# Optimization experiments

Measured on AMD Instinct MI355X. Metric: run time of the kernel, lower is better.

Reference implementation:

```python
import jax, jax.numpy as jnp
import numpy as np
import math

K_HISTORY = 32  # sliding-window length over GRU hidden states


def rotate_half(x):
    half = x.shape[-1] // 2
    return jnp.concatenate([-x[..., half:], x[..., :half]], axis=-1)


def setup_inputs() -> dict:
    key = jax.random.key(0)
    ks = jax.random.split(key, 8)
    B, MB, IN = 8, 512, 1024          # batch, max_bin, input_size (gru_hidden_size)
    EMB, H, KVH, HD, BS = 1024, 16, 4, 64, 16  # embed_dim, heads, kv_heads, head_dim, bin_size
    h = jax.random.normal(ks[0], (B, MB, IN), jnp.float32)
    # RoPE tables: rotate-half layout, theta repeated over both halves
    pos = jnp.arange(MB, dtype=jnp.float32)
    inv_freq = 1.0 / (10000.0 ** (jnp.arange(0, HD, 2, dtype=jnp.float32) / HD))
    theta = pos[:, None] * inv_freq[None, :]            # (MB, HD/2)
    theta = jnp.concatenate([theta, theta], axis=-1)    # (MB, HD)
    freqs_cos = jnp.cos(theta)
    freqs_sin = jnp.sin(theta)
    s = 0.02
    Wq = jax.random.normal(ks[1], (EMB, H * HD), jnp.float32) * s
    Wk = jax.random.normal(ks[2], (IN, KVH * HD), jnp.float32) * s
    Wv = jax.random.normal(ks[3], (IN, KVH * HD), jnp.float32) * s
    Wo = jax.random.normal(ks[4], (H * HD, EMB), jnp.float32) * s
    output_queries = jax.random.normal(ks[5], (BS, EMB), jnp.float32)
    Wr = jax.random.normal(ks[6], (EMB, 2), jnp.float32) * s
    br = jnp.zeros((2,), jnp.float32)
    return {"h": h, "freqs_cos": freqs_cos, "freqs_sin": freqs_sin,
            "Wq": Wq, "Wk": Wk, "Wv": Wv, "Wo": Wo,
            "output_queries": output_queries, "Wr": Wr, "br": br}


def reference(h, freqs_cos, freqs_sin, Wq, Wk, Wv, Wo, output_queries, Wr, br):
    B, MB, IN = h.shape
    HD = freqs_cos.shape[1]
    H = Wq.shape[1] // HD
    KVH = Wk.shape[1] // HD
    n_rep = H // KVH
    BS = output_queries.shape[0]
    K = K_HISTORY

    # sliding windows over bins: window t covers h[t-K+1 : t+1] (zero left-pad)
    h_padded = jnp.concatenate([jnp.zeros((B, K - 1, IN), h.dtype), h], axis=1)
    idx = jnp.arange(MB)[:, None] + jnp.arange(K)[None, :]   # (MB, K)
    h_win = h_padded[:, idx, :]                              # (B, MB, K, IN)

    k = (h_win @ Wk).reshape(B, MB, K, KVH, HD)
    v = (h_win @ Wv).reshape(B, MB, K, KVH, HD)

    # queries: shared learned output queries, identical across batch & bins
    q = (output_queries @ Wq).reshape(BS, H, HD)             # (BS, H, HD)
    # RoPE on Q only (is_decoder=True) at within-bin offsets 0..BS-1
    offs = jnp.arange(BS)
    cos = freqs_cos[offs][:, None, :]                        # (BS, 1, HD)
    sin = freqs_sin[offs][:, None, :]
    q = q * cos + rotate_half(q) * sin                       # (BS, H, HD)

    # GQA: repeat_interleave KV heads to H heads
    k = jnp.repeat(k, n_rep, axis=3)                         # (B, MB, K, H, HD)
    v = jnp.repeat(v, n_rep, axis=3)

    scores = jnp.einsum("qhd,bmkhd->bmhqk", q, k) / math.sqrt(HD)
    attn = jax.nn.softmax(scores, axis=-1)                   # (B, MB, H, BS, K)
    attn_out = jnp.einsum("bmhqk,bmkhd->bmqhd", attn, v)
    attn_out = attn_out.reshape(B, MB, BS, H * HD)

    z = attn_out @ Wo                                        # (B, MB, BS, EMB)
    vel = z @ Wr + br                                        # (B, MB, BS, 2)
    return vel.reshape(B, MB * BS, 2)
```

## Files before the change

kernel.cpp:

```cpp
#include <hip/hip_runtime.h>


typedef __attribute__((ext_vector_type(8))) short v8s;
typedef __attribute__((ext_vector_type(4))) float v4f;

#define OFF_WOR  0u
#define OFF_QR   2048u
#define OFF_WTH  18432u
#define OFF_WTL  182272u
#define OFF_S0   346112u
#define OFF_VW0  2574336u
#define OFF_AH   2852864u
#define OFF_AL   4950016u
#define SROW 544

__device__ __forceinline__ void split_bf16(float a, unsigned short& h, unsigned short& l) {
    const unsigned u = __float_as_uint(a);
    h = (unsigned short)(u >> 16);
    const float r = a - __uint_as_float(u & 0xFFFF0000u);
    unsigned v = __float_as_uint(r);
    v += 0x7FFFu + ((v >> 16) & 1u);
    l = (unsigned short)(v >> 16);
}

__global__ __launch_bounds__(256) void kP(
    const float* __restrict__ oq, const float* __restrict__ Wq,
    const float* __restrict__ fc, const float* __restrict__ fs,
    const float* __restrict__ Wo, const float* __restrict__ Wr,
    const float* __restrict__ hsrc,
    float* __restrict__ qr, float* __restrict__ Wor,
    float* __restrict__ S0, float* __restrict__ VW0,
    unsigned* __restrict__ wthu, unsigned* __restrict__ wtlu,
    unsigned short* __restrict__ Ahg, unsigned short* __restrict__ Alg)
{
    __shared__ float sm[2048];
    const int b = blockIdx.x, t = threadIdx.x;
    if (b >= 586) {
        const int base = (b - 586) * 2048 + t * 8;
        const float4 x0 = *(const float4*)(hsrc + base);
        const float4 x1 = *(const float4*)(hsrc + base + 4);
        const float af[8] = {x0.x, x0.y, x0.z, x0.w, x1.x, x1.y, x1.z, x1.w};
        v8s ah, al;
        #pragma unroll
        for (int j = 0; j < 8; ++j) {
            unsigned short hh, ll;
            split_bf16(af[j], hh, ll);
            ah[j] = (short)hh; al[j] = (short)ll;
        }
        *(v8s*)(Ahg + base) = ah;
        *(v8s*)(Alg + base) = al;
        return;
    }
    if (b < 256) {
        const int q = b >> 4, h = b & 15;
        #pragma unroll
        for (int j = 0; j < 4; ++j) sm[t + 256 * j] = oq[q * 1024 + t + 256 * j];
        __syncthreads();
        const int w = t >> 6, lane = t & 63;
        const float* wq = Wq + (size_t)(w * 256) * 1024 + h * 64 + lane;
        const float* os = sm + w * 256;
        float acc = 0.f;
        #pragma unroll 16
        for (int e = 0; e < 256; ++e) acc = fmaf(os[e], wq[(size_t)e * 1024], acc);
        sm[1024 + w * 64 + lane] = acc;
        __syncthreads();
        if (t < 64) {
            const int d = t, p = d ^ 32;
            const float a1 = sm[1024 + d] + sm[1088 + d] + sm[1152 + d] + sm[1216 + d];
            const float a2 = sm[1024 + p] + sm[1088 + p] + sm[1152 + p] + sm[1216 + p];
            const float c = fc[q * 64 + d], s = fs[q * 64 + d];
            const float rh = (d < 32) ? -a2 : a2;
            qr[q * 1024 + h * 64 + d] = fmaf(a1, c, rh * s);
        }
    } else if (b < 512) {
        #pragma unroll
        for (int j = 0; j < 8; ++j) sm[t + 256 * j] = Wr[t + 256 * j];
        __syncthreads();
        const int i = (b - 256) * 4 + (t >> 6);
        const int lane = t & 63;
        float a0 = 0.f, a1 = 0.f;
        const float* wo = Wo + (size_t)i * 1024 + lane;
        #pragma unroll
        for (int j = 0; j < 16; ++j) {
            const float w = wo[j * 64];
            const int e = lane + j * 64;
            a0 = fmaf(w, sm[2 * e], a0);
            a1 = fmaf(w, sm[2 * e + 1], a1);
        }
        #pragma unroll
        for (int w = 1; w < 64; w <<= 1) {
            a0 += __shfl_xor(a0, w, 64);
            a1 += __shfl_xor(a1, w, 64);
        }
        if (lane == 0) { Wor[i * 2] = a0; Wor[i * 2 + 1] = a1; }
    } else if (b < 584) {
        const int idx = (b - 512) * 256 + t;
        const float4 z = make_float4(0.f, 0.f, 0.f, 0.f);
        if (idx < 16384)  *(float4*)(S0  + (size_t)(idx >> 3) * SROW + (idx & 7) * 4) = z;
        else              *(float4*)(VW0 + (size_t)((idx - 16384) >> 3) * SROW + (idx & 7) * 4) = z;
    } else {
        unsigned* dst = (b == 584) ? wthu : wtlu;
        #pragma unroll
        for (int j = 0; j < 64; ++j) dst[147456 + t + 256 * j] = 0u;
    }
}

__global__ __launch_bounds__(256) void kW(
    const float* __restrict__ Wk, const float* __restrict__ Wv,
    const float* __restrict__ qr, const float* __restrict__ Wor,
    unsigned short* __restrict__ Wth, unsigned short* __restrict__ Wtl)
{
    __shared__ float As[16 * 68];
    __shared__ float Bt[72 * 68];
    const int b = blockIdx.x, t = threadIdx.x;
    const int g = b & 3, i0 = (b >> 2) * 16;
    #pragma unroll
    for (int jj = 0; jj < 16; ++jj) {
        const int i2 = t + 256 * jj;
        const int d = i2 & 63, col = i2 >> 6;
        Bt[col * 68 + d] = qr[(col >> 2) * 1024 + (g * 4 + (col & 3)) * 64 + d];
    }
    #pragma unroll
    for (int jj = 0; jj < 2; ++jj) {
        const int i2 = t + 256 * jj;
        const int d = i2 & 63, vc = i2 >> 6;
        Bt[(64 + vc) * 68 + d] = Wor[((g * 4 + (vc >> 1)) * 64 + d) * 2 + (vc & 1)];
    }
    {
        const int i = t >> 4, dc = (t & 15) * 4;
        *(float4*)&As[i * 68 + dc] = *(const float4*)(Wk + (size_t)(i0 + i) * 256 + g * 64 + dc);
    }
    __syncthreads();
    const int jc = t & 63, iq = t >> 6;
    {
        float o4[4] = {0.f, 0.f, 0.f, 0.f};
        #pragma unroll
        for (int dc = 0; dc < 16; ++dc) {
            const float4 bv = *(const float4*)&Bt[jc * 68 + dc * 4];
            #pragma unroll
            for (int r = 0; r < 4; ++r) {
                const float4 av = *(const float4*)&As[(iq * 4 + r) * 68 + dc * 4];
                o4[r] = fmaf(av.x, bv.x, o4[r]);
                o4[r] = fmaf(av.y, bv.y, o4[r]);
                o4[r] = fmaf(av.z, bv.z, o4[r]);
                o4[r] = fmaf(av.w, bv.w, o4[r]);
            }
        }
        const int j = (jc >> 2) * 16 + g * 4 + (jc & 3);
        #pragma unroll
        for (int r = 0; r < 4; ++r) {
            unsigned short hh, ll;
            split_bf16(o4[r] * 0.125f, hh, ll);
            Wth[(size_t)j * 1024 + i0 + iq * 4 + r] = hh;
            Wtl[(size_t)j * 1024 + i0 + iq * 4 + r] = ll;
        }
    }
    __syncthreads();
    {
        const int i = t >> 4, dc = (t & 15) * 4;
        *(float4*)&As[i * 68 + dc] = *(const float4*)(Wv + (size_t)(i0 + i) * 256 + g * 64 + dc);
    }
    __syncthreads();
    if (t < 128) {
        const int il = t >> 3, vc = t & 7;
        float acc = 0.f;
        #pragma unroll
        for (int dc = 0; dc < 16; ++dc) {
            const float4 av = *(const float4*)&As[il * 68 + dc * 4];
            const float4 bv = *(const float4*)&Bt[(64 + vc) * 68 + dc * 4];
            acc = fmaf(av.x, bv.x, acc);
            acc = fmaf(av.y, bv.y, acc);
            acc = fmaf(av.z, bv.z, acc);
            acc = fmaf(av.w, bv.w, acc);
        }
        const int j = 256 + (g * 4 + (vc >> 1)) * 2 + (vc & 1);
        unsigned short hh, ll;
        split_bf16(acc, hh, ll);
        Wth[(size_t)j * 1024 + i0 + il] = hh;
        Wtl[(size_t)j * 1024 + i0 + il] = ll;
    }
}

__global__ __launch_bounds__(256, 2) void k2(
    const unsigned short* __restrict__ Ahg, const unsigned short* __restrict__ Alg,
    const unsigned short* __restrict__ Wth, const unsigned short* __restrict__ Wtl,
    float* __restrict__ S0, float* __restrict__ VW0)
{
    __shared__ float red[4][64][68];
    const int m0 = blockIdx.x * 64;
    const int n0 = blockIdx.y * 64;
    const int t = threadIdx.x;
    const int w = t >> 6, lane = t & 63;
    const int l16 = lane & 15, quad = lane >> 4;

    const size_t aoff = (size_t)(m0 + l16) * 1024 + w * 256 + quad * 8;
    const size_t boff = (size_t)(n0 + l16) * 1024 + w * 256 + quad * 8;
    const unsigned short* pah = Ahg + aoff;
    const unsigned short* pal = Alg + aoff;
    const unsigned short* pbh = Wth + boff;
    const unsigned short* pbl = Wtl + boff;

    v4f acc[4][4];
    #pragma unroll
    for (int i = 0; i < 4; ++i)
        #pragma unroll
        for (int j = 0; j < 4; ++j) acc[i][j] = (v4f)(0.f);

    v8s fah[2][4], fal[2][4], fbh[2][4], fbl[2][4];
    #pragma unroll
    for (int s = 0; s < 4; ++s) {
        fah[0][s] = *(const v8s*)(pah + s * 16384);
        fal[0][s] = *(const v8s*)(pal + s * 16384);
        fbh[0][s] = *(const v8s*)(pbh + s * 16384);
        fbl[0][s] = *(const v8s*)(pbl + s * 16384);
    }
    #pragma unroll 8
    for (int it = 0; it < 8; ++it) {
        const int cur = it & 1, nxt = cur ^ 1;
        if (it < 7) {
            const int ko = (it + 1) * 32;
            #pragma unroll
            for (int s = 0; s < 4; ++s) {
                fah[nxt][s] = *(const v8s*)(pah + s * 16384 + ko);
                fal[nxt][s] = *(const v8s*)(pal + s * 16384 + ko);
                fbh[nxt][s] = *(const v8s*)(pbh + s * 16384 + ko);
                fbl[nxt][s] = *(const v8s*)(pbl + s * 16384 + ko);
            }
        }
        #pragma unroll
        for (int ms = 0; ms < 4; ++ms)
            #pragma unroll
            for (int ns = 0; ns < 4; ++ns) {
                acc[ms][ns] = __builtin_amdgcn_mfma_f32_16x16x32_bf16(fal[cur][ms], fbh[cur][ns], acc[ms][ns], 0, 0, 0);
                acc[ms][ns] = __builtin_amdgcn_mfma_f32_16x16x32_bf16(fah[cur][ms], fbl[cur][ns], acc[ms][ns], 0, 0, 0);
                acc[ms][ns] = __builtin_amdgcn_mfma_f32_16x16x32_bf16(fah[cur][ms], fbh[cur][ns], acc[ms][ns], 0, 0, 0);
            }
    }

    #pragma unroll
    for (int ms = 0; ms < 4; ++ms)
        #pragma unroll
        for (int ns = 0; ns < 4; ++ns)
            *(v4f*)&red[w][lane][(ms * 4 + ns) * 4] = acc[ms][ns];
    __syncthreads();
    #pragma unroll
    for (int ns = 0; ns < 4; ++ns) {
        const int j = n0 + ns * 16 + l16;
        if (j >= 288) continue;
        const int fo = w * 16 + ns * 4;
        const v4f s0 = *(const v4f*)&red[0][lane][fo];
        const v4f s1 = *(const v4f*)&red[1][lane][fo];
        const v4f s2 = *(const v4f*)&red[2][lane][fo];
        const v4f s3 = *(const v4f*)&red[3][lane][fo];
        const v4f sv = s0 + s1 + s2 + s3;
        const int m = m0 + w * 16 + quad * 4;
        const int bb = m >> 9, tt = m & 511;
        float* dst = (j < 256)
            ? S0  + (size_t)((bb * 16 + (j >> 4)) * 16 + (j & 15)) * SROW + 32 + tt
            : VW0 + (size_t)(bb * 32 + (j - 256)) * SROW + 32 + tt;
        *(float4*)dst = make_float4(sv[0], sv[1], sv[2], sv[3]);
    }
}

__global__ __launch_bounds__(256) void k3(
    const float* __restrict__ S, const float* __restrict__ VW,
    const float* __restrict__ brp, float* __restrict__ out)
{
    __shared__ float Es[16 * 164];
    __shared__ float EVs[32 * 164];
    const int b = blockIdx.x, q = blockIdx.y, qt = blockIdx.z;
    const int tbase = qt * 128;
    const int t = threadIdx.x;
    for (int idx = t; idx < 640; idx += 256) {
        const int h = idx / 40, g = idx - h * 40;
        const size_t off = (size_t)((b * 16 + q) * 16 + h) * SROW + tbase + g * 4;
        const float4 a = *(const float4*)(S + off);
        float4 e;
        e.x = __expf(a.x); e.y = __expf(a.y);
        e.z = __expf(a.z); e.w = __expf(a.w);
        *(float4*)(Es + h * 164 + g * 4) = e;
    }
    __syncthreads();
    for (int idx = t; idx < 1280; idx += 256) {
        const int hc = idx / 40, g = idx - hc * 40;
        const size_t off = (size_t)(b * 32 + hc) * SROW + tbase + g * 4;
        const float4 v0 = *(const float4*)(VW + off);
        const float4 e = *(const float4*)(Es + (hc >> 1) * 164 + g * 4);
        float4 rr;
        rr.x = e.x * v0.x; rr.y = e.y * v0.y;
        rr.z = e.z * v0.z; rr.w = e.w * v0.w;
        *(float4*)(EVs + hc * 164 + g * 4) = rr;
    }
    __syncthreads();
    const int h = t & 15, mg = t >> 4;
    const float* ep = Es + h * 164 + mg * 8;
    const float* e0 = EVs + (2 * h) * 164 + mg * 8;
    const float* e1 = EVs + (2 * h + 1) * 164 + mg * 8;
    float den = 0.f, n0s = 0.f, n1s = 0.f;
    #pragma unroll
    for (int s = 0; s < 32; ++s) {
        const int ss = 1 + ((s + 2 * h) & 31);
        den += ep[ss]; n0s += e0[ss]; n1s += e1[ss];
    }
    const float br0 = brp[0], br1 = brp[1];
    #pragma unroll
    for (int u = 0; u < 8; ++u) {
        const float inv = __builtin_amdgcn_rcpf(den);
        float c0 = n0s * inv, c1 = n1s * inv;
        #pragma unroll
        for (int w = 1; w < 16; w <<= 1) {
            c0 += __shfl_xor(c0, w, 64);
            c1 += __shfl_xor(c1, w, 64);
        }
        if (h == 0) {
            const int m = tbase + mg * 8 + u;
            float* o = out + (size_t)((b * 512 + m) * 16 + q) * 2;
            o[0] = c0 + br0;
            o[1] = c1 + br1;
        }
        if (u < 7) {
            den += ep[33 + u] - ep[1 + u];
            n0s += e0[33 + u] - e0[1 + u];
            n1s += e1[33 + u] - e1[1 + u];
        }
    }
}

extern "C" void kernel_launch(void* const* d_in, const int* in_sizes, int n_in,
                              void* d_out, int out_size, void* d_ws, size_t ws_size,
                              hipStream_t stream)
{
    (void)in_sizes; (void)n_in; (void)out_size; (void)ws_size;
    const float* h  = (const float*)d_in[0];
    const float* fc = (const float*)d_in[1];
    const float* fs = (const float*)d_in[2];
    const float* Wq = (const float*)d_in[3];
    const float* Wk = (const float*)d_in[4];
    const float* Wv = (const float*)d_in[5];
    const float* Wo = (const float*)d_in[6];
    const float* oq = (const float*)d_in[7];
    const float* Wr = (const float*)d_in[8];
    const float* br = (const float*)d_in[9];
    float* ws = (float*)d_ws;
    float* Wor  = ws + OFF_WOR;
    float* qr   = ws + OFF_QR;
    unsigned short* Wth = (unsigned short*)(ws + OFF_WTH);
    unsigned short* Wtl = (unsigned short*)(ws + OFF_WTL);
    float* S0   = ws + OFF_S0;
    float* VW0  = ws + OFF_VW0;
    unsigned short* Ahg = (unsigned short*)(ws + OFF_AH);
    unsigned short* Alg = (unsigned short*)(ws + OFF_AL);
    float* out = (float*)d_out;

    hipLaunchKernelGGL(kP, dim3(2634), dim3(256), 0, stream,
                       oq, Wq, fc, fs, Wo, Wr, h, qr, Wor, S0, VW0,
                       (unsigned*)Wth, (unsigned*)Wtl, Ahg, Alg);
    hipLaunchKernelGGL(kW, dim3(256), dim3(256), 0, stream, Wk, Wv, qr, Wor, Wth, Wtl);
    hipLaunchKernelGGL(k2, dim3(64, 5), dim3(256), 0, stream, Ahg, Alg, Wth, Wtl, S0, VW0);
    hipLaunchKernelGGL(k3, dim3(8, 16, 4), dim3(256), 0, stream, S0, VW0, br, out);
}
```

Baseline: 138.1 us.

## Pre-pack A and W operands into MFMA fragment layout and retile N to 48

The bf16 hi/lo split of h is now written in an MFMA-fragment-packed layout via an LDS transpose, and the fused weights are written in the same packed layout, so each lane in the GEMM issues fully contiguous 16-byte loads. The GEMM N tiling changes from 5 tiles of 64 (last one padded) to 6 tiles of 48, covering exactly 288 columns. This removes the wasted padded MFMA work and the zero-fill of the padding rows. The costs are an extra shared-memory staging pass in the pack kernel and a more complex index computation for the weight stores.

```diff
diff --git a/kernel.cpp b/kernel.cpp
--- a/kernel.cpp
+++ b/kernel.cpp
@@ -23,6 +23,11 @@
     l = (unsigned short)(v >> 16);
 }
 
+__device__ __forceinline__ size_t pidx(int j, int i) {
+    return (size_t)(j >> 4) * 16384 + (size_t)((i >> 5)) * 512
+         + (size_t)(((i >> 3) & 3) * 128 + (j & 15) * 8 + (i & 7));
+}
+
 __global__ __launch_bounds__(256) void kP(
     const float* __restrict__ oq, const float* __restrict__ Wq,
     const float* __restrict__ fc, const float* __restrict__ fs,
@@ -30,29 +35,48 @@
     const float* __restrict__ hsrc,
     float* __restrict__ qr, float* __restrict__ Wor,
     float* __restrict__ S0, float* __restrict__ VW0,
-    unsigned* __restrict__ wthu, unsigned* __restrict__ wtlu,
     unsigned short* __restrict__ Ahg, unsigned short* __restrict__ Alg)
 {
-    __shared__ float sm[2048];
+    __shared__ unsigned short Hs[2][16][520];
+    float* sm = (float*)&Hs[0][0][0];
     const int b = blockIdx.x, t = threadIdx.x;
-    if (b >= 586) {
-        const int base = (b - 586) * 2048 + t * 8;
-        const float4 x0 = *(const float4*)(hsrc + base);
-        const float4 x1 = *(const float4*)(hsrc + base + 4);
-        const float af[8] = {x0.x, x0.y, x0.z, x0.w, x1.x, x1.y, x1.z, x1.w};
-        v8s ah, al;
-        #pragma unroll
-        for (int j = 0; j < 8; ++j) {
-            unsigned short hh, ll;
-            split_bf16(af[j], hh, ll);
-            ah[j] = (short)hh; al[j] = (short)ll;
-        }
-        *(v8s*)(Ahg + base) = ah;
-        *(v8s*)(Alg + base) = al;
+    if (b < 512) {
+        const int mb = b >> 1, kseg = b & 1;
+        const int w = t >> 6, lane = t & 63;
+        #pragma unroll
+        for (int i = 0; i < 4; ++i) {
+            const int r = i * 4 + w;
+            const float* src = hsrc + (size_t)(mb * 16 + r) * 1024 + kseg * 512 + lane * 8;
+            const float4 x0 = *(const float4*)src;
+            const float4 x1 = *(const float4*)(src + 4);
+            const float af[8] = {x0.x, x0.y, x0.z, x0.w, x1.x, x1.y, x1.z, x1.w};
+            v8s hh, ll;
+            #pragma unroll
+            for (int j = 0; j < 8; ++j) {
+                unsigned short ah, al;
+                split_bf16(af[j], ah, al);
+                hh[j] = (short)ah; ll[j] = (short)al;
+            }
+            *(v8s*)&Hs[0][r][lane * 8] = hh;
+            *(v8s*)&Hs[1][r][lane * 8] = ll;
+        }
+        __syncthreads();
+        unsigned short* dh = Ahg + (size_t)mb * 16384 + kseg * 8192;
+        unsigned short* dl = Alg + (size_t)mb * 16384 + kseg * 8192;
+        const int l16 = lane & 15, quad = lane >> 4;
+        #pragma unroll
+        for (int i = 0; i < 4; ++i) {
+            const int kc = (i * 4 + w) * 32 + quad * 8;
+            const v8s hh = *(const v8s*)&Hs[0][l16][kc];
+            const v8s ll = *(const v8s*)&Hs[1][l16][kc];
+            *(v8s*)(dh + i * 2048 + t * 8) = hh;
+            *(v8s*)(dl + i * 2048 + t * 8) = ll;
+        }
         return;
     }
-    if (b < 256) {
-        const int q = b >> 4, h = b & 15;
+    if (b < 768) {
+        const int b2 = b - 512;
+        const int q = b2 >> 4, h = b2 & 15;
         #pragma unroll
         for (int j = 0; j < 4; ++j) sm[t + 256 * j] = oq[q * 1024 + t + 256 * j];
         __syncthreads();
@@ -72,11 +96,11 @@
             const float rh = (d < 32) ? -a2 : a2;
             qr[q * 1024 + h * 64 + d] = fmaf(a1, c, rh * s);
         }
-    } else if (b < 512) {
+    } else if (b < 1024) {
         #pragma unroll
         for (int j = 0; j < 8; ++j) sm[t + 256 * j] = Wr[t + 256 * j];
         __syncthreads();
-        const int i = (b - 256) * 4 + (t >> 6);
+        const int i = (b - 768) * 4 + (t >> 6);
         const int lane = t & 63;
         float a0 = 0.f, a1 = 0.f;
         const float* wo = Wo + (size_t)i * 1024 + lane;
@@ -93,15 +117,11 @@
             a1 += __shfl_xor(a1, w, 64);
         }
         if (lane == 0) { Wor[i * 2] = a0; Wor[i * 2 + 1] = a1; }
-    } else if (b < 584) {
-        const int idx = (b - 512) * 256 + t;
+    } else {
+        const int idx = (b - 1024) * 256 + t;
         const float4 z = make_float4(0.f, 0.f, 0.f, 0.f);
         if (idx < 16384)  *(float4*)(S0  + (size_t)(idx >> 3) * SROW + (idx & 7) * 4) = z;
         else              *(float4*)(VW0 + (size_t)((idx - 16384) >> 3) * SROW + (idx & 7) * 4) = z;
-    } else {
-        unsigned* dst = (b == 584) ? wthu : wtlu;
-        #pragma unroll
-        for (int j = 0; j < 64; ++j) dst[147456 + t + 256 * j] = 0u;
     }
 }
 
@@ -151,8 +171,9 @@
         for (int r = 0; r < 4; ++r) {
             unsigned short hh, ll;
             split_bf16(o4[r] * 0.125f, hh, ll);
-            Wth[(size_t)j * 1024 + i0 + iq * 4 + r] = hh;
-            Wtl[(size_t)j * 1024 + i0 + iq * 4 + r] = ll;
+            const size_t o = pidx(j, i0 + iq * 4 + r);
+            Wth[o] = hh;
+            Wtl[o] = ll;
         }
     }
     __syncthreads();
@@ -176,8 +197,9 @@
         const int j = 256 + (g * 4 + (vc >> 1)) * 2 + (vc & 1);
         unsigned short hh, ll;
         split_bf16(acc, hh, ll);
-        Wth[(size_t)j * 1024 + i0 + il] = hh;
-        Wtl[(size_t)j * 1024 + i0 + il] = ll;
+        const size_t o = pidx(j, i0 + il);
+        Wth[o] = hh;
+        Wtl[o] = ll;
     }
 }
 
@@ -186,31 +208,34 @@
     const unsigned short* __restrict__ Wth, const unsigned short* __restrict__ Wtl,
     float* __restrict__ S0, float* __restrict__ VW0)
 {
-    __shared__ float red[4][64][68];
+    __shared__ float red[4][64][52];
     const int m0 = blockIdx.x * 64;
-    const int n0 = blockIdx.y * 64;
+    const int by = blockIdx.y;
     const int t = threadIdx.x;
     const int w = t >> 6, lane = t & 63;
     const int l16 = lane & 15, quad = lane >> 4;
 
-    const size_t aoff = (size_t)(m0 + l16) * 1024 + w * 256 + quad * 8;
-    const size_t boff = (size_t)(n0 + l16) * 1024 + w * 256 + quad * 8;
-    const unsigned short* pah = Ahg + aoff;
-    const unsigned short* pal = Alg + aoff;
-    const unsigned short* pbh = Wth + boff;
-    const unsigned short* pbl = Wtl + boff;
-
-    v4f acc[4][4];
+    const size_t abase = (size_t)blockIdx.x * 4 * 16384 + (size_t)w * 8 * 512 + lane * 8;
+    const size_t bbase = (size_t)by * 3 * 16384 + (size_t)w * 8 * 512 + lane * 8;
+    const unsigned short* pah = Ahg + abase;
+    const unsigned short* pal = Alg + abase;
+    const unsigned short* pbh = Wth + bbase;
+    const unsigned short* pbl = Wtl + bbase;
+
+    v4f acc[4][3];
     #pragma unroll
     for (int i = 0; i < 4; ++i)
         #pragma unroll
-        for (int j = 0; j < 4; ++j) acc[i][j] = (v4f)(0.f);
-
-    v8s fah[2][4], fal[2][4], fbh[2][4], fbl[2][4];
+        for (int j = 0; j < 3; ++j) acc[i][j] = (v4f)(0.f);
+
+    v8s fah[2][4], fal[2][4], fbh[2][3], fbl[2][3];
     #pragma unroll
     for (int s = 0; s < 4; ++s) {
         fah[0][s] = *(const v8s*)(pah + s * 16384);
         fal[0][s] = *(const v8s*)(pal + s * 16384);
+    }
+    #pragma unroll
+    for (int s = 0; s < 3; ++s) {
         fbh[0][s] = *(const v8s*)(pbh + s * 16384);
         fbl[0][s] = *(const v8s*)(pbl + s * 16384);
     }
@@ -218,11 +243,14 @@
     for (int it = 0; it < 8; ++it) {
         const int cur = it & 1, nxt = cur ^ 1;
         if (it < 7) {
-            const int ko = (it + 1) * 32;
+            const int ko = (it + 1) * 512;
             #pragma unroll
             for (int s = 0; s < 4; ++s) {
                 fah[nxt][s] = *(const v8s*)(pah + s * 16384 + ko);
                 fal[nxt][s] = *(const v8s*)(pal + s * 16384 + ko);
+            }
+            #pragma unroll
+            for (int s = 0; s < 3; ++s) {
                 fbh[nxt][s] = *(const v8s*)(pbh + s * 16384 + ko);
                 fbl[nxt][s] = *(const v8s*)(pbl + s * 16384 + ko);
             }
@@ -230,7 +258,7 @@
         #pragma unroll
         for (int ms = 0; ms < 4; ++ms)
             #pragma unroll
-            for (int ns = 0; ns < 4; ++ns) {
+            for (int ns = 0; ns < 3; ++ns) {
                 acc[ms][ns] = __builtin_amdgcn_mfma_f32_16x16x32_bf16(fal[cur][ms], fbh[cur][ns], acc[ms][ns], 0, 0, 0);
                 acc[ms][ns] = __builtin_amdgcn_mfma_f32_16x16x32_bf16(fah[cur][ms], fbl[cur][ns], acc[ms][ns], 0, 0, 0);
                 acc[ms][ns] = __builtin_amdgcn_mfma_f32_16x16x32_bf16(fah[cur][ms], fbh[cur][ns], acc[ms][ns], 0, 0, 0);
@@ -240,14 +268,13 @@
     #pragma unroll
     for (int ms = 0; ms < 4; ++ms)
         #pragma unroll
-        for (int ns = 0; ns < 4; ++ns)
-            *(v4f*)&red[w][lane][(ms * 4 + ns) * 4] = acc[ms][ns];
-    __syncthreads();
-    #pragma unroll
-    for (int ns = 0; ns < 4; ++ns) {
-        const int j = n0 + ns * 16 + l16;
-        if (j >= 288) continue;
-        const int fo = w * 16 + ns * 4;
+        for (int ns = 0; ns < 3; ++ns)
+            *(v4f*)&red[w][lane][(ms * 3 + ns) * 4] = acc[ms][ns];
+    __syncthreads();
+    #pragma unroll
+    for (int ns = 0; ns < 3; ++ns) {
+        const int j = by * 48 + ns * 16 + l16;
+        const int fo = (w * 3 + ns) * 4;
         const v4f s0 = *(const v4f*)&red[0][lane][fo];
         const v4f s1 = *(const v4f*)&red[1][lane][fo];
         const v4f s2 = *(const v4f*)&red[2][lane][fo];
@@ -352,10 +379,9 @@
     unsigned short* Alg = (unsigned short*)(ws + OFF_AL);
     float* out = (float*)d_out;
 
-    hipLaunchKernelGGL(kP, dim3(2634), dim3(256), 0, stream,
-                       oq, Wq, fc, fs, Wo, Wr, h, qr, Wor, S0, VW0,
-                       (unsigned*)Wth, (unsigned*)Wtl, Ahg, Alg);
+    hipLaunchKernelGGL(kP, dim3(1096), dim3(256), 0, stream,
+                       oq, Wq, fc, fs, Wo, Wr, h, qr, Wor, S0, VW0, Ahg, Alg);
     hipLaunchKernelGGL(kW, dim3(256), dim3(256), 0, stream, Wk, Wv, qr, Wor, Wth, Wtl);
-    hipLaunchKernelGGL(k2, dim3(64, 5), dim3(256), 0, stream, Ahg, Alg, Wth, Wtl, S0, VW0);
+    hipLaunchKernelGGL(k2, dim3(64, 6), dim3(256), 0, stream, Ahg, Alg, Wth, Wtl, S0, VW0);
     hipLaunchKernelGGL(k3, dim3(8, 16, 4), dim3(256), 0, stream, S0, VW0, br, out);
 }
```

New measurement: 122.4 us. 11.3% less time.
